# Kernel optimization log

Hardware: AMD Instinct MI355X
Metric: run time of the kernel (lower is better)

Reference implementation:

```python
import jax, jax.numpy as jnp
import numpy as np
from jax import lax

B, T, C, H, HOR = 64, 2048, 64, 256, 96
BETA, THR = 0.9, 1.0


def setup_inputs() -> dict:
    key = jax.random.key(0)
    ks = jax.random.split(key, 10)
    s = lambda *sh: 1.0 / np.sqrt(sh[-1])
    return {
        "x": jax.random.normal(ks[0], (B, T, C), jnp.float32),
        "snn_w": jax.random.uniform(ks[1], (H, C), jnp.float32, -s(C), s(C)),
        "snn_b": jax.random.uniform(ks[2], (H,), jnp.float32, -s(C), s(C)),
        "gru_wih": jax.random.uniform(ks[3], (3 * H, C + H), jnp.float32, -s(H), s(H)),
        "gru_whh": jax.random.uniform(ks[4], (3 * H, H), jnp.float32, -s(H), s(H)),
        "gru_bih": jax.random.uniform(ks[5], (3 * H,), jnp.float32, -s(H), s(H)),
        "gru_bhh": jax.random.uniform(ks[6], (3 * H,), jnp.float32, -s(H), s(H)),
        "head_w": jax.random.uniform(ks[7], (HOR, H), jnp.float32, -s(H), s(H)),
        "head_b": jax.random.uniform(ks[8], (HOR,), jnp.float32, -s(H), s(H)),
    }


@jax.custom_vjp
def spike(x):
    return (x > 0).astype(x.dtype)

def _spike_fwd(x):
    return spike(x), x

def _spike_bwd(x, g):
    # snntorch ATan surrogate, alpha=2: grad = 1 / (1 + (pi*x)^2)
    return (g / (1.0 + (jnp.pi * x) ** 2),)

spike.defvjp(_spike_fwd, _spike_bwd)


def reference(x, snn_w, snn_b, gru_wih, gru_whh, gru_bih, gru_bhh, head_w, head_b):
    # Batched SNN input current across all timesteps: [B,T,H]
    cur = jnp.einsum("btc,hc->bth", x, snn_w) + snn_b

    def lif_step(mem, i_t):
        # reset computed from previous mem, detached (snntorch mem_reset)
        reset = lax.stop_gradient((mem > THR).astype(mem.dtype))
        mem_new = BETA * mem + i_t - reset * THR
        spk = spike(mem_new - THR)
        return mem_new, spk

    mem0 = jnp.zeros((B, H), x.dtype)
    _, spks = lax.scan(lif_step, mem0, cur.transpose(1, 0, 2))  # [T,B,H]

    h_comb = jnp.concatenate([x, spks.transpose(1, 0, 2)], axis=-1)  # [B,T,C+H]

    # GRU: precompute input gates for all timesteps
    gx = jnp.einsum("btc,gc->btg", h_comb, gru_wih) + gru_bih  # [B,T,3H]

    def gru_step(h, gx_t):
        gh = h @ gru_whh.T + gru_bhh
        xr, xz, xn = jnp.split(gx_t, 3, axis=-1)
        hr, hz, hn = jnp.split(gh, 3, axis=-1)
        r = jax.nn.sigmoid(xr + hr)
        z = jax.nn.sigmoid(xz + hz)
        n = jnp.tanh(xn + r * hn)
        h_new = (1.0 - z) * n + z * h
        return h_new, None

    h0 = jnp.zeros((B, H), x.dtype)
    hT, _ = lax.scan(gru_step, h0, gx.transpose(1, 0, 2))

    return hT @ head_w.T + head_b  # [B, HOR]
```

## Files before the change

kernel.cpp:

```cpp
#include <hip/hip_runtime.h>
#include <cstdint>
#include <cstddef>

#define B_   64
#define T_   2048
#define C_   64
#define H_   256
#define G3_  768
#define HOR_ 96

typedef _Float16 h2 __attribute__((ext_vector_type(2)));
typedef _Float16 h8 __attribute__((ext_vector_type(8)));
typedef _Float16 f16x8 __attribute__((ext_vector_type(8)));
typedef float f32x4 __attribute__((ext_vector_type(4)));

#define K1_TT 128
__global__ __launch_bounds__(256) void k_cur(const float* __restrict__ x,
                                             const float* __restrict__ w,
                                             const float* __restrict__ bias,
                                             float* __restrict__ cur,
                                             int* __restrict__ flags) {
  __shared__ float xs[K1_TT * C_];
  const int b = blockIdx.x;
  const int t0 = blockIdx.y * K1_TT;
  const int tid = threadIdx.x;

  if (b == 0 && blockIdx.y == 0) {
#pragma unroll
    for (int i = 0; i < 4; i++) flags[tid + i * 256] = 0;
  }

  const float4* xsrc = (const float4*)(x + ((size_t)b * T_ + t0) * C_);
  float4* xdst = (float4*)xs;
#pragma unroll
  for (int i = 0; i < (K1_TT * C_ / 4) / 256; i++)
    xdst[tid + i * 256] = xsrc[tid + i * 256];

  float wr[C_];
  const float4* wp = (const float4*)(w + (size_t)tid * C_);
#pragma unroll
  for (int q = 0; q < C_ / 4; q++) {
    float4 v = wp[q];
    wr[4 * q + 0] = v.x; wr[4 * q + 1] = v.y;
    wr[4 * q + 2] = v.z; wr[4 * q + 3] = v.w;
  }
  const float bb = bias[tid];
  __syncthreads();

  for (int t = 0; t < K1_TT; t++) {
    const float4* xrow = (const float4*)(xs + t * C_);
    float a0 = 0.f, a1 = 0.f;
#pragma unroll
    for (int q = 0; q < C_ / 4; q += 2) {
      float4 v0 = xrow[q];
      float4 v1 = xrow[q + 1];
      a0 += wr[4 * q + 0] * v0.x + wr[4 * q + 1] * v0.y +
            wr[4 * q + 2] * v0.z + wr[4 * q + 3] * v0.w;
      a1 += wr[4 * q + 4] * v1.x + wr[4 * q + 5] * v1.y +
            wr[4 * q + 6] * v1.z + wr[4 * q + 7] * v1.w;
    }
    cur[((size_t)b * T_ + t0 + t) * H_ + tid] = a0 + a1 + bb;
  }
}

__global__ __launch_bounds__(64) void k_lif(const float* __restrict__ cur,
                                            unsigned char* __restrict__ spk) {
  const int b = blockIdx.x >> 2;
  const int h = ((blockIdx.x & 3) << 6) + threadIdx.x;
  const float* cp = cur + (size_t)b * T_ * H_ + h;
  unsigned char* sp = spk + (size_t)b * T_ * H_ + h;
  float mem = 0.f;
#pragma unroll 32
  for (int t = 0; t < T_; t++) {
    float c = cp[(size_t)t * H_];
    float reset = (mem > 1.0f) ? 1.0f : 0.0f;
    mem = 0.9f * mem + c - reset;
    sp[(size_t)t * H_] = (mem > 1.0f) ? (unsigned char)1 : (unsigned char)0;
  }
}

#define GM 128
#define GN 128
#define AKP 40
#define CTP 136
#define DQ_ (0.0625f / (127.0f * 127.0f))
__global__ __launch_bounds__(512) void k_fused(
    const float* __restrict__ x, const unsigned char* __restrict__ spk,
    const float* __restrict__ wih, const float* __restrict__ bih,
    _Float16* __restrict__ gx, const float* __restrict__ whh,
    const float* __restrict__ bhh, const float* __restrict__ head_w,
    const float* __restrict__ head_b, float* __restrict__ out,
    int* __restrict__ flags) {
  alignas(16) __shared__ _Float16 Ah[GM * AKP];
  alignas(16) __shared__ _Float16 Bh[GN * AKP];
  alignas(16) __shared__ _Float16 Ct[GM * CTP];
  alignas(16) __shared__ int hq[2][64];
  __shared__ float hbuf32[H_];

  const int tid = threadIdx.x;
  const int lane = tid & 63;

  if (blockIdx.x >= 64) {
    const int pidx = blockIdx.x - 64;
    const int bb = pidx / 3;
    const int pp = pidx - bb * 3;
    const int wave = tid >> 6;
    const int ln = lane & 15;
    const int qd = lane >> 4;
    const int wm = (wave & 1) * 64;
    const int wn = ((wave >> 1) & 1) * 64;

    for (int mt = 0; mt < 16; mt++) {
      const int m0 = bb * 2048 + mt * 128;
      for (int nh = 0; nh < 2; nh++) {
        const int n0 = pp * 256 + nh * 128;
        f32x4 acc[4][4] = {};
        for (int kc = 0; kc < 10; kc++) {
          const int k0 = kc * 32;
          if (tid < 256) {
            if (k0 < 64) {
#pragma unroll
              for (int i = 0; i < 4; i++) {
                int idx = tid + i * 256;
                int r = idx >> 3;
                int c4 = (idx & 7) * 4;
                float4 v = *(const float4*)(x + (size_t)(m0 + r) * C_ + k0 + c4);
                h2 lo, hi;
                lo.x = (_Float16)v.x; lo.y = (_Float16)v.y;
                hi.x = (_Float16)v.z; hi.y = (_Float16)v.w;
                h2* d = (h2*)&Ah[r * AKP + c4];
                d[0] = lo; d[1] = hi;
              }
            } else {
#pragma unroll
              for (int i = 0; i < 4; i++) {
                int idx = tid + i * 256;
                int r = idx >> 3;
                int c4 = (idx & 7) * 4;
                uchar4 u = *(const uchar4*)(spk + (size_t)(m0 + r) * H_ + (k0 - 64) + c4);
                h2 lo, hi;
                lo.x = (_Float16)(int)u.x; lo.y = (_Float16)(int)u.y;
                hi.x = (_Float16)(int)u.z; hi.y = (_Float16)(int)u.w;
                h2* d = (h2*)&Ah[r * AKP + c4];
                d[0] = lo; d[1] = hi;
              }
            }
#pragma unroll
            for (int i = 0; i < 4; i++) {
              int idx = tid + i * 256;
              int r = idx >> 3;
              int c4 = (idx & 7) * 4;
              float4 v = *(const float4*)(wih + (size_t)(n0 + r) * 320 + k0 + c4);
              h2 lo, hi;
              lo.x = (_Float16)v.x; lo.y = (_Float16)v.y;
              hi.x = (_Float16)v.z; hi.y = (_Float16)v.w;
              h2* d = (h2*)&Bh[r * AKP + c4];
              d[0] = lo; d[1] = hi;
            }
          }
          __syncthreads();
          if (tid < 256) {
            f16x8 a[4], bbf[4];
#pragma unroll
            for (int mtl = 0; mtl < 4; mtl++)
              a[mtl] = *(const f16x8*)&Ah[(wm + mtl * 16 + ln) * AKP + qd * 8];
#pragma unroll
            for (int nt = 0; nt < 4; nt++)
              bbf[nt] = *(const f16x8*)&Bh[(wn + nt * 16 + ln) * AKP + qd * 8];
#pragma unroll
            for (int mtl = 0; mtl < 4; mtl++)
#pragma unroll
              for (int nt = 0; nt < 4; nt++)
                acc[mtl][nt] = __builtin_amdgcn_mfma_f32_16x16x32_f16(
                    a[mtl], bbf[nt], acc[mtl][nt], 0, 0, 0);
          }
          __syncthreads();
        }
        if (tid < 256) {
          float bias[4];
#pragma unroll
          for (int nt = 0; nt < 4; nt++) bias[nt] = bih[n0 + wn + nt * 16 + ln];
#pragma unroll
          for (int mtl = 0; mtl < 4; mtl++)
#pragma unroll
            for (int nt = 0; nt < 4; nt++) {
              int n = wn + nt * 16 + ln;
#pragma unroll
              for (int r = 0; r < 4; r++) {
                int m = wm + mtl * 16 + qd * 4 + r;
                Ct[m * CTP + n] = (_Float16)(acc[mtl][nt][r] + bias[nt]);
              }
            }
        }
        __syncthreads();
        if (tid < 256) {
#pragma unroll
          for (int i = 0; i < 8; i++) {
            int idx = tid + i * 256;
            int r = idx >> 4;
            int c = (idx & 15) * 8;
            *(h8*)(gx + (size_t)(m0 + r) * G3_ + n0 + c) = *(const h8*)&Ct[r * CTP + c];
          }
        }
        __syncthreads();
      }
      if (tid == 0)
        __hip_atomic_fetch_add(&flags[bb * 16 + mt], 1, __ATOMIC_RELEASE,
                               __HIP_MEMORY_SCOPE_AGENT);
    }
    return;
  }

  const int b = blockIdx.x;
  const int wave = tid >> 6;
  const int j = wave * 32 + (lane >> 1);
  const int kq = lane & 1;
  const int k0 = kq * 128;

  int wr[32], wz[32], wn[32];
  {
    const float qs = 2032.0f;
    const float4* p0 = (const float4*)(whh + (size_t)j * H_ + k0);
    const float4* p1 = (const float4*)(whh + (size_t)(H_ + j) * H_ + k0);
    const float4* p2 = (const float4*)(whh + (size_t)(2 * H_ + j) * H_ + k0);
#pragma unroll
    for (int q = 0; q < 32; q++) {
      float4 a = p0[q];
      wr[q] = ((int)rintf(a.x * qs) & 255) | (((int)rintf(a.y * qs) & 255) << 8) |
              (((int)rintf(a.z * qs) & 255) << 16) | (((int)rintf(a.w * qs) & 255) << 24);
      float4 c = p1[q];
      wz[q] = ((int)rintf(c.x * qs) & 255) | (((int)rintf(c.y * qs) & 255) << 8) |
              (((int)rintf(c.z * qs) & 255) << 16) | (((int)rintf(c.w * qs) & 255) << 24);
      float4 d = p2[q];
      wn[q] = ((int)rintf(d.x * qs) & 255) | (((int)rintf(d.y * qs) & 255) << 8) |
              (((int)rintf(d.z * qs) & 255) << 16) | (((int)rintf(d.w * qs) & 255) << 24);
    }
  }
  const float br_ = bhh[j], bz_ = bhh[H_ + j], bn_ = bhh[2 * H_ + j];

  if (tid < 128) ((int*)hq)[tid] = 0;
  float hj = 0.f;
  __syncthreads();

  const _Float16* gxb = gx + (size_t)b * T_ * G3_;
  int p = 0;
  for (int mt = 0; mt < 16; mt++) {
    if (tid == 0) {
      while (__hip_atomic_load(&flags[b * 16 + mt], __ATOMIC_ACQUIRE,
                               __HIP_MEMORY_SCOPE_AGENT) < 3)
        __builtin_amdgcn_s_sleep(8);
    }
    __syncthreads();

    const _Float16* gc = gxb + (size_t)mt * 128 * G3_;
    _Float16 pr = gc[j], pz = gc[H_ + j], pn = gc[2 * H_ + j];

    for (int tt = 0; tt < 128; tt++) {
      float xr = (float)pr, xz = (float)pz, xn = (float)pn;
      if (tt < 127) {
        const _Float16* g = gc + (size_t)(tt + 1) * G3_;
        pr = g[j]; pz = g[H_ + j]; pn = g[2 * H_ + j];
      }

      const int* hb = &hq[p][kq * 32];
      int ar = 0, az = 0, an = 0;
#pragma unroll
      for (int g4 = 0; g4 < 4; g4++) {
#pragma unroll
        for (int cc = 0; cc < 2; cc++) {
          int c = g4 * 2 + cc;
          int4 hv = *(const int4*)(hb + c * 4);
#pragma unroll
          for (int i = 0; i < 4; i++) {
            int h4 = (i == 0) ? hv.x : (i == 1) ? hv.y : (i == 2) ? hv.z : hv.w;
            int wi = c * 4 + i;
            ar = __builtin_amdgcn_sdot4(wr[wi], h4, ar, false);
            az = __builtin_amdgcn_sdot4(wz[wi], h4, az, false);
            an = __builtin_amdgcn_sdot4(wn[wi], h4, an, false);
          }
        }
        __builtin_amdgcn_sched_barrier(2 | 4 | 16 | 32 | 64);
      }
      ar += __shfl_xor(ar, 1, 64);
      az += __shfl_xor(az, 1, 64);
      an += __shfl_xor(an, 1, 64);

      float r = 1.f / (1.f + __expf(-(xr + (float)ar * DQ_ + br_)));
      float z = 1.f / (1.f + __expf(-(xz + (float)az * DQ_ + bz_)));
      float pre = xn + r * ((float)an * DQ_ + bn_);
      float e = __expf(2.f * pre);
      float n = 1.f - 2.f / (e + 1.f);
      hj = (1.f - z) * n + z * hj;

      if (kq == 0) ((char*)hq[p ^ 1])[j] = (char)(int)rintf(hj * 127.0f);
      p ^= 1;
      __syncthreads();
    }
  }

  if (kq == 0) hbuf32[j] = hj;
  __syncthreads();

  if (tid < HOR_) {
    const float4* hw = (const float4*)(head_w + (size_t)tid * H_);
    const float4* hv4 = (const float4*)hbuf32;
    float acc = head_b[tid];
#pragma unroll
    for (int q = 0; q < H_ / 4; q++) {
      float4 w4 = hw[q];
      float4 v4 = hv4[q];
      acc += w4.x * v4.x + w4.y * v4.y + w4.z * v4.z + w4.w * v4.w;
    }
    out[(size_t)b * HOR_ + tid] = acc;
  }
}

extern "C" void kernel_launch(void* const* d_in, const int* in_sizes, int n_in,
                              void* d_out, int out_size, void* d_ws, size_t ws_size,
                              hipStream_t stream) {
  const float* x      = (const float*)d_in[0];
  const float* snn_w  = (const float*)d_in[1];
  const float* snn_b  = (const float*)d_in[2];
  const float* wih    = (const float*)d_in[3];
  const float* whh    = (const float*)d_in[4];
  const float* bih    = (const float*)d_in[5];
  const float* bhh    = (const float*)d_in[6];
  const float* head_w = (const float*)d_in[7];
  const float* head_b = (const float*)d_in[8];
  float* out = (float*)d_out;

  char* ws = (char*)d_ws;
  _Float16* gx = (_Float16*)ws;
  float* cur = (float*)ws;
  unsigned char* spk = (unsigned char*)(ws + (size_t)201326592);
  int* flags = (int*)(ws + (size_t)234881024);

  k_cur<<<dim3(B_, T_ / K1_TT), 256, 0, stream>>>(x, snn_w, snn_b, cur, flags);
  k_lif<<<dim3(256), 64, 0, stream>>>(cur, spk);
  k_fused<<<dim3(256), 512, 0, stream>>>(x, spk, wih, bih, gx, whh, bhh,
                                         head_w, head_b, out, flags);
}
```

Baseline: 1.971 ms.

## Shrink fused kernel to 256 threads, one hidden unit per thread in GRU

The fused kernel drops from 512 to 256 threads per block. In the recurrent GRU blocks each thread now owns a full hidden unit with all 256 quantized weights per gate in registers (192 ints), so the cross-lane shuffle reduction is gone. Two interleaved accumulators per gate shorten the dot-product dependency chains. The cost is much higher register pressure and twice the sequential dot-product work per thread on every timestep. This may lengthen the serial critical path even though the shuffles and idle GEMM threads are removed.

```diff
diff --git a/kernel.cpp b/kernel.cpp
--- a/kernel.cpp
+++ b/kernel.cpp
@@ -84,7 +84,7 @@
 #define AKP 40
 #define CTP 136
 #define DQ_ (0.0625f / (127.0f * 127.0f))
-__global__ __launch_bounds__(512) void k_fused(
+__global__ __launch_bounds__(256) void k_fused(
     const float* __restrict__ x, const unsigned char* __restrict__ spk,
     const float* __restrict__ wih, const float* __restrict__ bih,
     _Float16* __restrict__ gx, const float* __restrict__ whh,
@@ -117,49 +117,47 @@
         f32x4 acc[4][4] = {};
         for (int kc = 0; kc < 10; kc++) {
           const int k0 = kc * 32;
-          if (tid < 256) {
-            if (k0 < 64) {
-#pragma unroll
-              for (int i = 0; i < 4; i++) {
-                int idx = tid + i * 256;
-                int r = idx >> 3;
-                int c4 = (idx & 7) * 4;
-                float4 v = *(const float4*)(x + (size_t)(m0 + r) * C_ + k0 + c4);
-                h2 lo, hi;
-                lo.x = (_Float16)v.x; lo.y = (_Float16)v.y;
-                hi.x = (_Float16)v.z; hi.y = (_Float16)v.w;
-                h2* d = (h2*)&Ah[r * AKP + c4];
-                d[0] = lo; d[1] = hi;
-              }
-            } else {
-#pragma unroll
-              for (int i = 0; i < 4; i++) {
-                int idx = tid + i * 256;
-                int r = idx >> 3;
-                int c4 = (idx & 7) * 4;
-                uchar4 u = *(const uchar4*)(spk + (size_t)(m0 + r) * H_ + (k0 - 64) + c4);
-                h2 lo, hi;
-                lo.x = (_Float16)(int)u.x; lo.y = (_Float16)(int)u.y;
-                hi.x = (_Float16)(int)u.z; hi.y = (_Float16)(int)u.w;
-                h2* d = (h2*)&Ah[r * AKP + c4];
-                d[0] = lo; d[1] = hi;
-              }
-            }
+          if (k0 < 64) {
 #pragma unroll
             for (int i = 0; i < 4; i++) {
               int idx = tid + i * 256;
               int r = idx >> 3;
               int c4 = (idx & 7) * 4;
-              float4 v = *(const float4*)(wih + (size_t)(n0 + r) * 320 + k0 + c4);
+              float4 v = *(const float4*)(x + (size_t)(m0 + r) * C_ + k0 + c4);
               h2 lo, hi;
               lo.x = (_Float16)v.x; lo.y = (_Float16)v.y;
               hi.x = (_Float16)v.z; hi.y = (_Float16)v.w;
-              h2* d = (h2*)&Bh[r * AKP + c4];
+              h2* d = (h2*)&Ah[r * AKP + c4];
+              d[0] = lo; d[1] = hi;
+            }
+          } else {
+#pragma unroll
+            for (int i = 0; i < 4; i++) {
+              int idx = tid + i * 256;
+              int r = idx >> 3;
+              int c4 = (idx & 7) * 4;
+              uchar4 u = *(const uchar4*)(spk + (size_t)(m0 + r) * H_ + (k0 - 64) + c4);
+              h2 lo, hi;
+              lo.x = (_Float16)(int)u.x; lo.y = (_Float16)(int)u.y;
+              hi.x = (_Float16)(int)u.z; hi.y = (_Float16)(int)u.w;
+              h2* d = (h2*)&Ah[r * AKP + c4];
               d[0] = lo; d[1] = hi;
             }
           }
+#pragma unroll
+          for (int i = 0; i < 4; i++) {
+            int idx = tid + i * 256;
+            int r = idx >> 3;
+            int c4 = (idx & 7) * 4;
+            float4 v = *(const float4*)(wih + (size_t)(n0 + r) * 320 + k0 + c4);
+            h2 lo, hi;
+            lo.x = (_Float16)v.x; lo.y = (_Float16)v.y;
+            hi.x = (_Float16)v.z; hi.y = (_Float16)v.w;
+            h2* d = (h2*)&Bh[r * AKP + c4];
+            d[0] = lo; d[1] = hi;
+          }
           __syncthreads();
-          if (tid < 256) {
+          {
             f16x8 a[4], bbf[4];
 #pragma unroll
             for (int mtl = 0; mtl < 4; mtl++)
@@ -176,7 +174,7 @@
           }
           __syncthreads();
         }
-        if (tid < 256) {
+        {
           float bias[4];
 #pragma unroll
           for (int nt = 0; nt < 4; nt++) bias[nt] = bih[n0 + wn + nt * 16 + ln];
@@ -193,14 +191,12 @@
             }
         }
         __syncthreads();
-        if (tid < 256) {
-#pragma unroll
-          for (int i = 0; i < 8; i++) {
-            int idx = tid + i * 256;
-            int r = idx >> 4;
-            int c = (idx & 15) * 8;
-            *(h8*)(gx + (size_t)(m0 + r) * G3_ + n0 + c) = *(const h8*)&Ct[r * CTP + c];
-          }
+#pragma unroll
+        for (int i = 0; i < 8; i++) {
+          int idx = tid + i * 256;
+          int r = idx >> 4;
+          int c = (idx & 15) * 8;
+          *(h8*)(gx + (size_t)(m0 + r) * G3_ + n0 + c) = *(const h8*)&Ct[r * CTP + c];
         }
         __syncthreads();
       }
@@ -212,19 +208,16 @@
   }
 
   const int b = blockIdx.x;
-  const int wave = tid >> 6;
-  const int j = wave * 32 + (lane >> 1);
-  const int kq = lane & 1;
-  const int k0 = kq * 128;
-
-  int wr[32], wz[32], wn[32];
+  const int j = tid;
+
+  int wr[64], wz[64], wn[64];
   {
     const float qs = 2032.0f;
-    const float4* p0 = (const float4*)(whh + (size_t)j * H_ + k0);
-    const float4* p1 = (const float4*)(whh + (size_t)(H_ + j) * H_ + k0);
-    const float4* p2 = (const float4*)(whh + (size_t)(2 * H_ + j) * H_ + k0);
-#pragma unroll
-    for (int q = 0; q < 32; q++) {
+    const float4* p0 = (const float4*)(whh + (size_t)j * H_);
+    const float4* p1 = (const float4*)(whh + (size_t)(H_ + j) * H_);
+    const float4* p2 = (const float4*)(whh + (size_t)(2 * H_ + j) * H_);
+#pragma unroll
+    for (int q = 0; q < 64; q++) {
       float4 a = p0[q];
       wr[q] = ((int)rintf(a.x * qs) & 255) | (((int)rintf(a.y * qs) & 255) << 8) |
               (((int)rintf(a.z * qs) & 255) << 16) | (((int)rintf(a.w * qs) & 255) << 24);
@@ -262,28 +255,32 @@
         pr = g[j]; pz = g[H_ + j]; pn = g[2 * H_ + j];
       }
 
-      const int* hb = &hq[p][kq * 32];
-      int ar = 0, az = 0, an = 0;
+      const int* hb = hq[p];
+      int ar0 = 0, ar1 = 0, az0 = 0, az1 = 0, an0 = 0, an1 = 0;
 #pragma unroll
       for (int g4 = 0; g4 < 4; g4++) {
 #pragma unroll
-        for (int cc = 0; cc < 2; cc++) {
-          int c = g4 * 2 + cc;
+        for (int cc = 0; cc < 4; cc++) {
+          int c = g4 * 4 + cc;
           int4 hv = *(const int4*)(hb + c * 4);
 #pragma unroll
           for (int i = 0; i < 4; i++) {
             int h4 = (i == 0) ? hv.x : (i == 1) ? hv.y : (i == 2) ? hv.z : hv.w;
             int wi = c * 4 + i;
-            ar = __builtin_amdgcn_sdot4(wr[wi], h4, ar, false);
-            az = __builtin_amdgcn_sdot4(wz[wi], h4, az, false);
-            an = __builtin_amdgcn_sdot4(wn[wi], h4, an, false);
+            if (wi & 1) {
+              ar1 = __builtin_amdgcn_sdot4(wr[wi], h4, ar1, false);
+              az1 = __builtin_amdgcn_sdot4(wz[wi], h4, az1, false);
+              an1 = __builtin_amdgcn_sdot4(wn[wi], h4, an1, false);
+            } else {
+              ar0 = __builtin_amdgcn_sdot4(wr[wi], h4, ar0, false);
+              az0 = __builtin_amdgcn_sdot4(wz[wi], h4, az0, false);
+              an0 = __builtin_amdgcn_sdot4(wn[wi], h4, an0, false);
+            }
           }
         }
         __builtin_amdgcn_sched_barrier(2 | 4 | 16 | 32 | 64);
       }
-      ar += __shfl_xor(ar, 1, 64);
-      az += __shfl_xor(az, 1, 64);
-      an += __shfl_xor(an, 1, 64);
+      int ar = ar0 + ar1, az = az0 + az1, an = an0 + an1;
 
       float r = 1.f / (1.f + __expf(-(xr + (float)ar * DQ_ + br_)));
       float z = 1.f / (1.f + __expf(-(xz + (float)az * DQ_ + bz_)));
@@ -292,13 +289,13 @@
       float n = 1.f - 2.f / (e + 1.f);
       hj = (1.f - z) * n + z * hj;
 
-      if (kq == 0) ((char*)hq[p ^ 1])[j] = (char)(int)rintf(hj * 127.0f);
+      ((char*)hq[p ^ 1])[j] = (char)(int)rintf(hj * 127.0f);
       p ^= 1;
       __syncthreads();
     }
   }
 
-  if (kq == 0) hbuf32[j] = hj;
+  hbuf32[j] = hj;
   __syncthreads();
 
   if (tid < HOR_) {
@@ -337,6 +334,6 @@
 
   k_cur<<<dim3(B_, T_ / K1_TT), 256, 0, stream>>>(x, snn_w, snn_b, cur, flags);
   k_lif<<<dim3(256), 64, 0, stream>>>(cur, spk);
-  k_fused<<<dim3(256), 512, 0, stream>>>(x, spk, wih, bih, gx, whh, bhh,
+  k_fused<<<dim3(256), 256, 0, stream>>>(x, spk, wih, bih, gx, whh, bhh,
                                          head_w, head_b, out, flags);
 }
```

Measured after the change: 1.852 ms (median of 2 runs). 1.06x faster.
